# Performance work log

Measured on AMD Instinct MI355X. Metric: run time of the kernel, lower is better.

The kernel has to match this reference:

```python
import jax, jax.numpy as jnp
import numpy as np

AUTHOR_FAMILY_CODET = jnp.array([0, 1, 2, 1, 3, 3], dtype=jnp.int32)
MARGIN = 0.3

def setup_inputs() -> dict:
    key = jax.random.key(0)
    k1, k2 = jax.random.split(key)
    B, D = 8192, 256
    embeddings = jax.random.normal(k1, (B, D), dtype=jnp.float32)
    labels = jax.random.randint(k2, (B,), 0, 6, dtype=jnp.int64)
    return {"embeddings": embeddings, "labels": labels}

def reference(embeddings, labels):
    B = embeddings.shape[0]
    # family lookup; labels out of table range would be -1 (cannot happen here
    # since fill_max == table length, but kept for faithfulness)
    lab = labels.astype(jnp.int32)
    table_len = AUTHOR_FAMILY_CODET.shape[0]
    fam = jnp.where(lab < table_len,
                    AUTHOR_FAMILY_CODET[jnp.clip(lab, 0, table_len - 1)],
                    -1)
    # cosine distance matrix [B, B]
    emb_norm = embeddings / jnp.linalg.norm(embeddings, axis=-1, keepdims=True)
    dist = 1.0 - emb_norm @ emb_norm.T
    valid_row = fam >= 0                                   # [B]
    same = (fam[:, None] == fam[None, :]) & valid_row[:, None]
    same = same & ~jnp.eye(B, dtype=bool)                  # exclude self
    diff = (fam[:, None] != fam[None, :]) & valid_row[None, :] & valid_row[:, None]
    d_pos = jnp.max(jnp.where(same, dist, -2.0), axis=1)   # hardest positive
    d_neg = jnp.min(jnp.where(diff, dist, 4.0), axis=1)    # hardest negative
    valid = valid_row & jnp.any(same, axis=1) & jnp.any(diff, axis=1)
    triplet = jax.nn.relu(d_pos - d_neg + MARGIN) * valid.astype(dist.dtype)
    count = jnp.sum(valid.astype(jnp.int32))
    return jnp.sum(triplet) / jnp.maximum(count, 1).astype(dist.dtype)
```

## Files before the change

### kernel.cpp

```cpp
#include <hip/hip_runtime.h>


typedef __attribute__((ext_vector_type(8))) _Float16 half8;
typedef __attribute__((ext_vector_type(4))) float floatx4;
typedef __attribute__((ext_vector_type(4))) unsigned short ushort4v;

constexpr int D = 256;
#define MARGIN 0.3f
#define FAM_PACKED 111240

static __device__ __forceinline__ void ld_g2l16(const unsigned short* g,
                                                unsigned short* l) {
  __builtin_amdgcn_global_load_lds(
      (const __attribute__((address_space(1))) unsigned int*)(const void*)g,
      (__attribute__((address_space(3))) unsigned int*)(void*)l, 16, 0, 0);
}

static __device__ __forceinline__ unsigned packmm(float mn, float mx) {
  unsigned lo = __builtin_bit_cast(unsigned short, (_Float16)mn);
  unsigned hi = __builtin_bit_cast(unsigned short, (_Float16)mx);
  return lo | (hi << 16);
}
static __device__ __forceinline__ float mmlo(unsigned p) {
  return (float)__builtin_bit_cast(_Float16, (unsigned short)(p & 0xFFFF));
}
static __device__ __forceinline__ float mmhi(unsigned p) {
  return (float)__builtin_bit_cast(_Float16, (unsigned short)(p >> 16));
}

__global__ __launch_bounds__(256) void prep_kernel(
    const float* __restrict__ E, const int* __restrict__ labels,
    unsigned short* __restrict__ Eh, int* __restrict__ fam,
    float* __restrict__ sumAcc, int* __restrict__ cntAcc,
    int* __restrict__ doneCnt, int B) {
  if (blockIdx.x == 0 && threadIdx.x == 0) {
    sumAcc[0] = 0.0f; cntAcc[0] = 0; doneCnt[0] = 0;
  }
  int wave = blockIdx.x * 4 + (threadIdx.x >> 6);
  int lane = threadIdx.x & 63;
  int nw   = gridDim.x * 4;
  for (int row = wave; row < B; row += nw) {
    float4 v = *(const float4*)&E[(long)row * D + lane * 4];
    float s = v.x * v.x + v.y * v.y + v.z * v.z + v.w * v.w;
#pragma unroll
    for (int o = 1; o < 64; o <<= 1) s += __shfl_xor(s, o);
    float rn = 1.0f / sqrtf(s);
    ushort4v o4;
    o4.x = __builtin_bit_cast(unsigned short, (_Float16)(v.x * rn));
    o4.y = __builtin_bit_cast(unsigned short, (_Float16)(v.y * rn));
    o4.z = __builtin_bit_cast(unsigned short, (_Float16)(v.z * rn));
    o4.w = __builtin_bit_cast(unsigned short, (_Float16)(v.w * rn));
    *(ushort4v*)&Eh[(long)row * D + lane * 4] = o4;
    if (lane == 0) {
      int lab = labels[row];
      int labc = lab < 0 ? 0 : (lab > 5 ? 5 : lab);
      fam[row] = (lab < 6) ? ((FAM_PACKED >> (3 * labc)) & 7) : -1;
    }
  }
}

__global__ __launch_bounds__(256) void gram_kernel(
    const unsigned short* __restrict__ Eh, const int* __restrict__ fam,
    unsigned* __restrict__ part, int nt, int nTasks) {
  __shared__ unsigned short Bs[2][64 * 256];
  __shared__ unsigned colS[2][4][64];

  const int tid = threadIdx.x;
  const int w = tid >> 6, l = tid & 63;
  const int m = l & 15, q = l >> 4;
  const int half = w & 1;

  int srcRel[8];
#pragma unroll
  for (int t = 0; t < 8; ++t) {
    int c = w * 512 + t * 64 + l;
    int row = c >> 5, ch = c & 31;
    srcRel[t] = row * D + ((ch ^ (row & 7)) << 3);
  }

  const int t0 = (int)(((long)blockIdx.x * nTasks) / gridDim.x);
  const int t1 = (int)(((long)(blockIdx.x + 1) * nTasks) / gridDim.x);

  int rb = 0;
  while ((rb + 1) * (nt - rb) <= t0) ++rb;
  int ct = 2 * rb + (t0 - rb * (nt - rb + 1));

  half8 apan[8][2];
  int famv;
  {
    const int r0w = rb * 128 + w * 32;
#pragma unroll
    for (int ks = 0; ks < 8; ++ks)
#pragma unroll
      for (int mi = 0; mi < 2; ++mi)
        apan[ks][mi] = *(const half8*)
            &Eh[(long)(r0w + mi * 16 + m) * D + ks * 32 + q * 8];
    famv = fam[r0w + (l & 31)];
  }

  {
    const unsigned short* src = Eh + (long)ct * 64 * D;
#pragma unroll
    for (int t = 0; t < 8; ++t)
      ld_g2l16(src + srcRel[t], &Bs[0][(w * 512 + t * 64) * 8]);
  }

  int p = 0;
  int mct = -1, mrb = -1;
#pragma unroll 1
  for (int f = t0; f < t1; ++f) {
    __syncthreads();

    if (mct >= 0 && l < 16) {
      const int sb = (f - 1) & 1;
      const int col = w * 16 + l;
      float mn = 4.0f, mx = -4.0f;
#pragma unroll
      for (int ww = 0; ww < 4; ++ww) {
        unsigned pk = colS[sb][ww][col];
        mn = fminf(mn, mmlo(pk));
        mx = fmaxf(mx, mmhi(pk));
      }
      part[((long)mct * nt + mrb) * 64 + col] = packmm(mn, mx);
    }

    const int rt64 = 2 * rb + (w >> 1);
    const bool doit = (rt64 <= ct);
    const int sb = f & 1;
    floatx4 acc[2][4];
#pragma unroll
    for (int mi = 0; mi < 2; ++mi)
#pragma unroll
      for (int nj = 0; nj < 4; ++nj) acc[mi][nj] = (floatx4)0.0f;

    if (doit) {
      const unsigned short* bufp = &Bs[p][0];
#pragma unroll
      for (int ks = 0; ks < 8; ++ks) {
        half8 b[4];
#pragma unroll
        for (int nj = 0; nj < 4; ++nj) {
          int row = nj * 16 + m;
          b[nj] = *(const half8*)
              &bufp[row * 256 + (((ks * 4 + q) ^ (m & 7)) << 3)];
        }
#pragma unroll
        for (int mi = 0; mi < 2; ++mi)
#pragma unroll
          for (int nj = 0; nj < 4; ++nj)
            acc[mi][nj] = __builtin_amdgcn_mfma_f32_16x16x32_f16(
                apan[ks][mi], b[nj], acc[mi][nj], 0, 0, 0);
      }
    }

    int nrb = rb, nct = ct + 1;
    if (nct == nt) { ++nrb; nct = 2 * nrb; }
    if (f + 1 < t1) {
      const unsigned short* src = Eh + (long)nct * 64 * D;
#pragma unroll
      for (int t = 0; t < 8; ++t)
        ld_g2l16(src + srcRel[t], &Bs[p ^ 1][(w * 512 + t * 64) * 8]);
    }

    if (doit) {
      const int famcv = fam[ct * 64 + l];
      int famR[8], famC[4];
#pragma unroll
      for (int mi = 0; mi < 2; ++mi)
#pragma unroll
        for (int r = 0; r < 4; ++r)
          famR[mi * 4 + r] = __shfl(famv, mi * 16 + q * 4 + r);
#pragma unroll
      for (int nj = 0; nj < 4; ++nj) famC[nj] = __shfl(famcv, nj * 16 + m);

      float rMin[8], rMax[8], cMin[4], cMax[4];
#pragma unroll
      for (int i = 0; i < 8; ++i) { rMin[i] = 4.0f; rMax[i] = -4.0f; }
#pragma unroll
      for (int j = 0; j < 4; ++j) { cMin[j] = 4.0f; cMax[j] = -4.0f; }

#pragma unroll
      for (int mi = 0; mi < 2; ++mi)
#pragma unroll
        for (int nj = 0; nj < 4; ++nj)
#pragma unroll
          for (int r = 0; r < 4; ++r) {
            float d = acc[mi][nj][r];
            bool same = (famR[mi * 4 + r] == famC[nj]);
            float ds = same ? d : 4.0f;
            float dd = same ? -4.0f : d;
            rMin[mi * 4 + r] = fminf(rMin[mi * 4 + r], ds);
            rMax[mi * 4 + r] = fmaxf(rMax[mi * 4 + r], dd);
            cMin[nj] = fminf(cMin[nj], ds);
            cMax[nj] = fmaxf(cMax[nj], dd);
          }

#pragma unroll
      for (int o = 1; o < 16; o <<= 1)
#pragma unroll
        for (int i = 0; i < 8; ++i) {
          rMin[i] = fminf(rMin[i], __shfl_xor(rMin[i], o));
          rMax[i] = fmaxf(rMax[i], __shfl_xor(rMax[i], o));
        }
      if (m == 0) {
        unsigned* dst = part + ((long)rt64 * nt + ct) * 64;
#pragma unroll
        for (int mi = 0; mi < 2; ++mi)
#pragma unroll
          for (int r = 0; r < 4; ++r)
            dst[half * 32 + mi * 16 + q * 4 + r] =
                packmm(rMin[mi * 4 + r], rMax[mi * 4 + r]);
      }
#pragma unroll
      for (int o = 16; o < 64; o <<= 1)
#pragma unroll
        for (int j = 0; j < 4; ++j) {
          cMin[j] = fminf(cMin[j], __shfl_xor(cMin[j], o));
          cMax[j] = fmaxf(cMax[j], __shfl_xor(cMax[j], o));
        }
      if (q == 0) {
        const bool real = (rt64 < ct);
#pragma unroll
        for (int nj = 0; nj < 4; ++nj)
          colS[sb][w][nj * 16 + m] =
              real ? packmm(cMin[nj], cMax[nj]) : packmm(4.0f, -4.0f);
      }
    } else {
      if (q == 0)
#pragma unroll
        for (int nj = 0; nj < 4; ++nj)
          colS[sb][w][nj * 16 + m] = packmm(4.0f, -4.0f);
    }

    mct = ct; mrb = rb;
    if (f + 1 < t1 && nrb != rb) {
      const int r0w = nrb * 128 + w * 32;
#pragma unroll
      for (int ks = 0; ks < 8; ++ks)
#pragma unroll
        for (int mi = 0; mi < 2; ++mi)
          apan[ks][mi] = *(const half8*)
              &Eh[(long)(r0w + mi * 16 + m) * D + ks * 32 + q * 8];
      famv = fam[r0w + (l & 31)];
    }
    rb = nrb; ct = nct; p ^= 1;
  }
  __syncthreads();
  if (l < 16) {
    const int sb = (t1 - 1) & 1;
    const int col = w * 16 + l;
    float mn = 4.0f, mx = -4.0f;
#pragma unroll
    for (int ww = 0; ww < 4; ++ww) {
      unsigned pk = colS[sb][ww][col];
      mn = fminf(mn, mmlo(pk));
      mx = fmaxf(mx, mmhi(pk));
    }
    part[((long)mct * nt + mrb) * 64 + col] = packmm(mn, mx);
  }
}

__global__ __launch_bounds__(256) void reduce_kernel(
    const unsigned* __restrict__ part, float* __restrict__ sumAcc,
    int* __restrict__ cntAcc, int* __restrict__ doneCnt,
    float* __restrict__ out, int B, int nt) {
  int gid = blockIdx.x * 256 + threadIdx.x;
  int row = gid >> 2;
  int c   = gid & 3;
  int rt = row >> 6, rl = row & 63;
  const unsigned* base = part + ((long)rt * nt) * 64 + rl;
  float mn = 4.0f, mx = -4.0f;
  for (int k = rt + c; k < nt; k += 4) {
    unsigned pk = base[(long)k * 64];
    mn = fminf(mn, mmlo(pk));
    mx = fmaxf(mx, mmhi(pk));
  }
  if (rt >= 1) {
    int rbmax = rt >> 1;
    for (int k = c; k <= rbmax; k += 4) {
      unsigned pk = base[(long)k * 64];
      mn = fminf(mn, mmlo(pk));
      mx = fmaxf(mx, mmhi(pk));
    }
  }
#pragma unroll
  for (int o = 1; o < 4; o <<= 1) {
    mn = fminf(mn, __shfl_xor(mn, o));
    mx = fmaxf(mx, __shfl_xor(mx, o));
  }
  float loss = 0.0f;
  int cc = 0;
  if (c == 0 && mn < 3.0f && mx > -3.0f) {
    loss = fmaxf(mx - mn + MARGIN, 0.0f);
    cc = 1;
  }
#pragma unroll
  for (int o = 1; o < 64; o <<= 1) {
    loss += __shfl_xor(loss, o);
    cc   += __shfl_xor(cc, o);
  }
  __shared__ float ls[4];
  __shared__ int   cs[4];
  if ((threadIdx.x & 63) == 0) {
    ls[threadIdx.x >> 6] = loss;
    cs[threadIdx.x >> 6] = cc;
  }
  __syncthreads();
  if (threadIdx.x == 0) {
    atomicAdd(sumAcc, ls[0] + ls[1] + ls[2] + ls[3]);
    atomicAdd(cntAcc, cs[0] + cs[1] + cs[2] + cs[3]);
    __threadfence();
    int old = atomicAdd(doneCnt, 1);
    if (old == (int)gridDim.x - 1) {
      float S = atomicAdd(sumAcc, 0.0f);
      int   C = atomicAdd(cntAcc, 0);
      out[0] = S / (float)(C > 0 ? C : 1);
    }
  }
}

extern "C" void kernel_launch(void* const* d_in, const int* in_sizes, int n_in,
                              void* d_out, int out_size, void* d_ws, size_t ws_size,
                              hipStream_t stream) {
  const float* E      = (const float*)d_in[0];
  const int*   labels = (const int*)d_in[1];
  float*       out    = (float*)d_out;
  const int B  = in_sizes[1];
  const int nt = B / 64;
  const int RB = nt / 2;
  const int nTasks = RB * (nt - RB + 1);

  unsigned short* Eh = (unsigned short*)d_ws;
  int* fam           = (int*)(Eh + (size_t)B * D);
  unsigned* part     = (unsigned*)(fam + B);
  float* sumAcc      = (float*)(part + (size_t)nt * nt * 64);
  int* cntAcc        = (int*)(sumAcc + 1);
  int* doneCnt       = cntAcc + 1;

  prep_kernel<<<dim3(256), 256, 0, stream>>>(E, labels, Eh, fam,
                                             sumAcc, cntAcc, doneCnt, B);
  gram_kernel<<<dim3(512), 256, 0, stream>>>(Eh, fam, part, nt, nTasks);
  reduce_kernel<<<dim3(B * 4 / 256), 256, 0, stream>>>(part, sumAcc, cntAcc,
                                                       doneCnt, out, B, nt);
}
```

Baseline: 127.6 us.

## Split K staging into halves and accumulate row extrema across tasks in registers

Stages each 64-column B tile in two 128-wide K halves through a smaller LDS buffer. This halves shared memory per block and overlaps the next tile's load with the second half's MFMAs. Row min/max now stay in registers across all tasks of a row block and are written once per block into a slot-based partial array, instead of after every tile. The reduce kernel becomes one thread per row scanning 96 sentinel-filled slots, which needs an extra memset and an added barrier per iteration.

```diff
diff --git a/kernel.cpp b/kernel.cpp
--- a/kernel.cpp
+++ b/kernel.cpp
@@ -6,8 +6,10 @@
 typedef __attribute__((ext_vector_type(4))) unsigned short ushort4v;
 
 constexpr int D = 256;
+constexpr int NSLOT = 96;
 #define MARGIN 0.3f
 #define FAM_PACKED 111240
+#define SENT 0x7E7E7E7Eu
 
 static __device__ __forceinline__ void ld_g2l16(const unsigned short* g,
                                                 unsigned short* l) {
@@ -61,22 +63,23 @@
 
 __global__ __launch_bounds__(256) void gram_kernel(
     const unsigned short* __restrict__ Eh, const int* __restrict__ fam,
-    unsigned* __restrict__ part, int nt, int nTasks) {
-  __shared__ unsigned short Bs[2][64 * 256];
+    unsigned* __restrict__ part, int nt, int nTasks, int B) {
+  __shared__ unsigned short Bs[2][64 * 128];
   __shared__ unsigned colS[2][4][64];
 
   const int tid = threadIdx.x;
   const int w = tid >> 6, l = tid & 63;
   const int m = l & 15, q = l >> 4;
-  const int half = w & 1;
-
-  int srcRel[8];
-#pragma unroll
-  for (int t = 0; t < 8; ++t) {
-    int c = w * 512 + t * 64 + l;
-    int row = c >> 5, ch = c & 31;
-    srcRel[t] = row * D + ((ch ^ (row & 7)) << 3);
-  }
+
+  int srcRel[4];
+#pragma unroll
+  for (int rnd = 0; rnd < 4; ++rnd) {
+    int c_lin = rnd * 256 + tid;
+    int row = c_lin >> 4;
+    int ch = (c_lin & 15) ^ (row & 7);
+    srcRel[rnd] = row * D + ch * 8;
+  }
+  const int ldsW = w * 512;
 
   const int t0 = (int)(((long)blockIdx.x * nTasks) / gridDim.x);
   const int t1 = (int)(((long)(blockIdx.x + 1) * nTasks) / gridDim.x);
@@ -98,20 +101,24 @@
     famv = fam[r0w + (l & 31)];
   }
 
+  float rMin[8], rMax[8];
+#pragma unroll
+  for (int i = 0; i < 8; ++i) { rMin[i] = 4.0f; rMax[i] = -4.0f; }
+  const int rowSlot = 64 + (blockIdx.x & 31);
+
   {
     const unsigned short* src = Eh + (long)ct * 64 * D;
 #pragma unroll
-    for (int t = 0; t < 8; ++t)
-      ld_g2l16(src + srcRel[t], &Bs[0][(w * 512 + t * 64) * 8]);
-  }
-
-  int p = 0;
+    for (int rnd = 0; rnd < 4; ++rnd)
+      ld_g2l16(src + srcRel[rnd], &Bs[0][rnd * 2048 + ldsW]);
+  }
+
   int mct = -1, mrb = -1;
 #pragma unroll 1
   for (int f = t0; f < t1; ++f) {
     __syncthreads();
 
-    if (mct >= 0 && l < 16) {
+    if (mct >= 0 && mct != 2 * mrb && l < 16) {
       const int sb = (f - 1) & 1;
       const int col = w * 16 + l;
       float mn = 4.0f, mx = -4.0f;
@@ -121,12 +128,17 @@
         mn = fminf(mn, mmlo(pk));
         mx = fmaxf(mx, mmhi(pk));
       }
-      part[((long)mct * nt + mrb) * 64 + col] = packmm(mn, mx);
+      part[(long)mrb * B + mct * 64 + col] = packmm(mn, mx);
     }
 
     const int rt64 = 2 * rb + (w >> 1);
     const bool doit = (rt64 <= ct);
-    const int sb = f & 1;
+    const unsigned short* Bsrc = Eh + (long)ct * 64 * D;
+
+#pragma unroll
+    for (int rnd = 0; rnd < 4; ++rnd)
+      ld_g2l16(Bsrc + srcRel[rnd] + 128, &Bs[1][rnd * 2048 + ldsW]);
+
     floatx4 acc[2][4];
 #pragma unroll
     for (int mi = 0; mi < 2; ++mi)
@@ -134,15 +146,14 @@
       for (int nj = 0; nj < 4; ++nj) acc[mi][nj] = (floatx4)0.0f;
 
     if (doit) {
-      const unsigned short* bufp = &Bs[p][0];
-#pragma unroll
-      for (int ks = 0; ks < 8; ++ks) {
+#pragma unroll
+      for (int ks = 0; ks < 4; ++ks) {
         half8 b[4];
 #pragma unroll
         for (int nj = 0; nj < 4; ++nj) {
           int row = nj * 16 + m;
           b[nj] = *(const half8*)
-              &bufp[row * 256 + (((ks * 4 + q) ^ (m & 7)) << 3)];
+              &Bs[0][row * 128 + (((ks * 4 + q) ^ (m & 7)) << 3)];
         }
 #pragma unroll
         for (int mi = 0; mi < 2; ++mi)
@@ -153,16 +164,36 @@
       }
     }
 
+    __syncthreads();
+
     int nrb = rb, nct = ct + 1;
     if (nct == nt) { ++nrb; nct = 2 * nrb; }
     if (f + 1 < t1) {
-      const unsigned short* src = Eh + (long)nct * 64 * D;
-#pragma unroll
-      for (int t = 0; t < 8; ++t)
-        ld_g2l16(src + srcRel[t], &Bs[p ^ 1][(w * 512 + t * 64) * 8]);
-    }
-
+      const unsigned short* nsrc = Eh + (long)nct * 64 * D;
+#pragma unroll
+      for (int rnd = 0; rnd < 4; ++rnd)
+        ld_g2l16(nsrc + srcRel[rnd], &Bs[0][rnd * 2048 + ldsW]);
+    }
+
+    const int sb = f & 1;
     if (doit) {
+#pragma unroll
+      for (int ks = 0; ks < 4; ++ks) {
+        half8 b[4];
+#pragma unroll
+        for (int nj = 0; nj < 4; ++nj) {
+          int row = nj * 16 + m;
+          b[nj] = *(const half8*)
+              &Bs[1][row * 128 + (((ks * 4 + q) ^ (m & 7)) << 3)];
+        }
+#pragma unroll
+        for (int mi = 0; mi < 2; ++mi)
+#pragma unroll
+          for (int nj = 0; nj < 4; ++nj)
+            acc[mi][nj] = __builtin_amdgcn_mfma_f32_16x16x32_f16(
+                apan[4 + ks][mi], b[nj], acc[mi][nj], 0, 0, 0);
+      }
+
       const int famcv = fam[ct * 64 + l];
       int famR[8], famC[4];
 #pragma unroll
@@ -173,9 +204,7 @@
 #pragma unroll
       for (int nj = 0; nj < 4; ++nj) famC[nj] = __shfl(famcv, nj * 16 + m);
 
-      float rMin[8], rMax[8], cMin[4], cMax[4];
-#pragma unroll
-      for (int i = 0; i < 8; ++i) { rMin[i] = 4.0f; rMax[i] = -4.0f; }
+      float cMin[4], cMax[4];
 #pragma unroll
       for (int j = 0; j < 4; ++j) { cMin[j] = 4.0f; cMax[j] = -4.0f; }
 
@@ -196,22 +225,6 @@
           }
 
 #pragma unroll
-      for (int o = 1; o < 16; o <<= 1)
-#pragma unroll
-        for (int i = 0; i < 8; ++i) {
-          rMin[i] = fminf(rMin[i], __shfl_xor(rMin[i], o));
-          rMax[i] = fmaxf(rMax[i], __shfl_xor(rMax[i], o));
-        }
-      if (m == 0) {
-        unsigned* dst = part + ((long)rt64 * nt + ct) * 64;
-#pragma unroll
-        for (int mi = 0; mi < 2; ++mi)
-#pragma unroll
-          for (int r = 0; r < 4; ++r)
-            dst[half * 32 + mi * 16 + q * 4 + r] =
-                packmm(rMin[mi * 4 + r], rMax[mi * 4 + r]);
-      }
-#pragma unroll
       for (int o = 16; o < 64; o <<= 1)
 #pragma unroll
         for (int j = 0; j < 4; ++j) {
@@ -233,7 +246,26 @@
     }
 
     mct = ct; mrb = rb;
+
     if (f + 1 < t1 && nrb != rb) {
+#pragma unroll
+      for (int o = 1; o < 16; o <<= 1)
+#pragma unroll
+        for (int i = 0; i < 8; ++i) {
+          rMin[i] = fminf(rMin[i], __shfl_xor(rMin[i], o));
+          rMax[i] = fmaxf(rMax[i], __shfl_xor(rMax[i], o));
+        }
+      if (m == 0) {
+        unsigned* dst = part + (long)rowSlot * B + rb * 128 + w * 32;
+#pragma unroll
+        for (int mi = 0; mi < 2; ++mi)
+#pragma unroll
+          for (int r = 0; r < 4; ++r)
+            dst[mi * 16 + q * 4 + r] =
+                packmm(rMin[mi * 4 + r], rMax[mi * 4 + r]);
+      }
+#pragma unroll
+      for (int i = 0; i < 8; ++i) { rMin[i] = 4.0f; rMax[i] = -4.0f; }
       const int r0w = nrb * 128 + w * 32;
 #pragma unroll
       for (int ks = 0; ks < 8; ++ks)
@@ -243,10 +275,11 @@
               &Eh[(long)(r0w + mi * 16 + m) * D + ks * 32 + q * 8];
       famv = fam[r0w + (l & 31)];
     }
-    rb = nrb; ct = nct; p ^= 1;
-  }
+    rb = nrb; ct = nct;
+  }
+
   __syncthreads();
-  if (l < 16) {
+  if (mct >= 0 && mct != 2 * mrb && l < 16) {
     const int sb = (t1 - 1) & 1;
     const int col = w * 16 + l;
     float mn = 4.0f, mx = -4.0f;
@@ -256,41 +289,41 @@
       mn = fminf(mn, mmlo(pk));
       mx = fmaxf(mx, mmhi(pk));
     }
-    part[((long)mct * nt + mrb) * 64 + col] = packmm(mn, mx);
+    part[(long)mrb * B + mct * 64 + col] = packmm(mn, mx);
+  }
+#pragma unroll
+  for (int o = 1; o < 16; o <<= 1)
+#pragma unroll
+    for (int i = 0; i < 8; ++i) {
+      rMin[i] = fminf(rMin[i], __shfl_xor(rMin[i], o));
+      rMax[i] = fmaxf(rMax[i], __shfl_xor(rMax[i], o));
+    }
+  if (m == 0) {
+    unsigned* dst = part + (long)rowSlot * B + mrb * 128 + w * 32;
+#pragma unroll
+    for (int mi = 0; mi < 2; ++mi)
+#pragma unroll
+      for (int r = 0; r < 4; ++r)
+        dst[mi * 16 + q * 4 + r] = packmm(rMin[mi * 4 + r], rMax[mi * 4 + r]);
   }
 }
 
 __global__ __launch_bounds__(256) void reduce_kernel(
     const unsigned* __restrict__ part, float* __restrict__ sumAcc,
     int* __restrict__ cntAcc, int* __restrict__ doneCnt,
-    float* __restrict__ out, int B, int nt) {
-  int gid = blockIdx.x * 256 + threadIdx.x;
-  int row = gid >> 2;
-  int c   = gid & 3;
-  int rt = row >> 6, rl = row & 63;
-  const unsigned* base = part + ((long)rt * nt) * 64 + rl;
+    float* __restrict__ out, int B) {
+  int r = blockIdx.x * 256 + threadIdx.x;
   float mn = 4.0f, mx = -4.0f;
-  for (int k = rt + c; k < nt; k += 4) {
-    unsigned pk = base[(long)k * 64];
-    mn = fminf(mn, mmlo(pk));
-    mx = fmaxf(mx, mmhi(pk));
-  }
-  if (rt >= 1) {
-    int rbmax = rt >> 1;
-    for (int k = c; k <= rbmax; k += 4) {
-      unsigned pk = base[(long)k * 64];
+  for (int k = 0; k < NSLOT; ++k) {
+    unsigned pk = part[(long)k * B + r];
+    if (pk != SENT) {
       mn = fminf(mn, mmlo(pk));
       mx = fmaxf(mx, mmhi(pk));
     }
   }
-#pragma unroll
-  for (int o = 1; o < 4; o <<= 1) {
-    mn = fminf(mn, __shfl_xor(mn, o));
-    mx = fmaxf(mx, __shfl_xor(mx, o));
-  }
   float loss = 0.0f;
   int cc = 0;
-  if (c == 0 && mn < 3.0f && mx > -3.0f) {
+  if (mn < 3.0f && mx > -3.0f) {
     loss = fmaxf(mx - mn + MARGIN, 0.0f);
     cc = 1;
   }
@@ -333,13 +366,14 @@
   unsigned short* Eh = (unsigned short*)d_ws;
   int* fam           = (int*)(Eh + (size_t)B * D);
   unsigned* part     = (unsigned*)(fam + B);
-  float* sumAcc      = (float*)(part + (size_t)nt * nt * 64);
+  float* sumAcc      = (float*)(part + (size_t)NSLOT * B);
   int* cntAcc        = (int*)(sumAcc + 1);
   int* doneCnt       = cntAcc + 1;
 
   prep_kernel<<<dim3(256), 256, 0, stream>>>(E, labels, Eh, fam,
                                              sumAcc, cntAcc, doneCnt, B);
-  gram_kernel<<<dim3(512), 256, 0, stream>>>(Eh, fam, part, nt, nTasks);
-  reduce_kernel<<<dim3(B * 4 / 256), 256, 0, stream>>>(part, sumAcc, cntAcc,
-                                                       doneCnt, out, B, nt);
-}
+  hipMemsetAsync(part, 0x7E, (size_t)NSLOT * B * sizeof(unsigned), stream);
+  gram_kernel<<<dim3(512), 256, 0, stream>>>(Eh, fam, part, nt, nTasks, B);
+  reduce_kernel<<<dim3(B / 256), 256, 0, stream>>>(part, sumAcc, cntAcc,
+                                                   doneCnt, out, B);
+}
```

Result: slower. 135.4 us (+6.1%).
